# Kernel tuning notes

Hardware: AMD Instinct MI355X
Metric: run time of the kernel (lower is better)

Reference implementation:

```python
import jax, jax.numpy as jnp
import numpy as np

N_QUBITS = 6
BLOCKS = 3
LATENT = 3
DIM = 1 << N_QUBITS  # 64, state-vector size
BATCH = 131072
INP_DIM = 6  # must equal N_QUBITS (repo applies linear_pre to the n_qubits-dim recon)

# Wire 0 is the most-significant qubit (PennyLane convention).
_idx = np.arange(DIM)
BITS = ((_idx[:, None] >> (N_QUBITS - 1 - np.arange(N_QUBITS))) & 1)  # (64, 6)
# Chain of CZ(k, k+1): all diagonal, fold into one sign vector per block.
CZ_SIGN = jnp.asarray(np.prod(1 - 2 * (BITS[:, :-1] * BITS[:, 1:]), axis=1).astype(np.float32))  # (64,)
Z_SIGNS = jnp.asarray((1 - 2 * BITS).astype(np.float32))  # (64, 6): <Z_k> signs per basis state


def _apply_1q(state, U, wire):
    # state: (B, 64) complex64; U: (2,2) complex64 acting on `wire`
    B = state.shape[0]
    s = state.reshape(B, 1 << wire, 2, 1 << (N_QUBITS - 1 - wire))
    s = jnp.einsum('ij,bxjy->bxiy', U, s)
    return s.reshape(B, DIM)


def _circuit(amps, weights, n_out):
    # AmplitudeEmbedding with normalize=True (x was already unit-normed in torch; idempotent)
    norm = jnp.linalg.norm(amps, axis=1, keepdims=True)
    state = (amps / norm).astype(jnp.complex64)  # (B, 64)
    for j in range(BLOCKS):
        for k in range(N_QUBITS):
            tx = weights[j, k, 0]
            tz = weights[j, k, 1]
            c = jnp.cos(0.5 * tx).astype(jnp.complex64)
            s = jnp.sin(0.5 * tx).astype(jnp.complex64)
            em = jnp.exp(-0.5j * tz).astype(jnp.complex64)
            ep = jnp.exp(0.5j * tz).astype(jnp.complex64)
            # Fused U = RZ(tz) @ RX(tx)
            U = jnp.stack([jnp.stack([em * c, -1j * em * s]),
                           jnp.stack([-1j * ep * s, ep * c])])
            state = _apply_1q(state, U, k)
        state = state * CZ_SIGN  # all CZ gates of the block, fused
    probs = state.real ** 2 + state.imag ** 2  # (B, 64)
    return probs @ Z_SIGNS[:, :n_out]  # expval(PauliZ(k)) for k < n_out


def setup_inputs() -> dict:
    key = jax.random.key(0)
    k1, k2, k3, k4, k5 = jax.random.split(key, 5)
    x = jax.random.normal(k1, (BATCH, INP_DIM), dtype=jnp.float32)
    bound = 1.0 / np.sqrt(INP_DIM)
    W_pre = jax.random.uniform(k2, (DIM, INP_DIM), minval=-bound, maxval=bound, dtype=jnp.float32)
    b_pre = jax.random.uniform(k3, (DIM,), minval=-bound, maxval=bound, dtype=jnp.float32)
    enc_w = jax.random.normal(k4, (BLOCKS, N_QUBITS, 3), dtype=jnp.float32) * 0.01
    dec_w = jax.random.normal(k5, (BLOCKS, N_QUBITS, 3), dtype=jnp.float32) * 0.01
    return {'x': x, 'W_pre': W_pre, 'b_pre': b_pre, 'enc_w': enc_w, 'dec_w': dec_w}


def reference(x, W_pre, b_pre, enc_w, dec_w):
    h = jnp.tanh(x @ W_pre.T + b_pre)                     # (B, 64)
    latent = _circuit(h, enc_w, LATENT)                    # (B, 3)
    padded = jnp.zeros((x.shape[0], DIM), jnp.float32).at[:, :LATENT].set(latent)
    recon = _circuit(padded, dec_w, N_QUBITS)              # (B, 6)
    reconstructed = jnp.tanh(recon @ W_pre.T + b_pre)      # (B, 64)
    return reconstructed, latent
```

## Files before the change

kernel.cpp:

```cpp
#include <hip/hip_runtime.h>

#define BATCH 131072

typedef float v2f __attribute__((ext_vector_type(2)));


__device__ __forceinline__ float fast_tanh(float v) {
    float e = __expf(2.0f * v);
    return 1.0f - 2.0f / (e + 1.0f);
}

template <int CTRL>
__device__ __forceinline__ float dppf(float v) {
    return __int_as_float(__builtin_amdgcn_update_dpp(
        0, __float_as_int(v), CTRL, 0xF, 0xF, true));
}
#define DPP_XOR1 0xB1
#define DPP_XOR2 0x4E

__device__ __forceinline__ v2f swap2(v2f v) { return __builtin_shufflevector(v, v, 1, 0); }

__global__ __launch_bounds__(256) void prep_kernel(const float* __restrict__ enc_w,
                                                   const float* __restrict__ dec_w,
                                                   const float* __restrict__ Wp,
                                                   const float* __restrict__ bp,
                                                   float* __restrict__ ws) {
    __shared__ float gt[18][8];
    __shared__ float Sr[64][8];
    __shared__ float Si[64][8];
    __shared__ float sA[36];
    const int t = threadIdx.x;

    if (t < 18) {
        float tx = dec_w[t * 3 + 0];
        float tz = dec_w[t * 3 + 1];
        float c = cosf(0.5f * tx), s = sinf(0.5f * tx);
        float ch = cosf(0.5f * tz), sh = sinf(0.5f * tz);
        gt[t][0] = c * ch;  gt[t][1] = -c * sh;
        gt[t][2] = -s * sh; gt[t][3] = -s * ch;
        gt[t][4] = s * sh;  gt[t][5] = -s * ch;
        gt[t][6] = c * ch;  gt[t][7] = c * sh;
    }

    const int cl = t & 7;
    const int pr = t >> 3;
    float* fSr = &Sr[0][0];
    float* fSi = &Si[0][0];
    for (int f = t; f < 512; f += 256) {
        int r = f >> 3, c = f & 7;
        fSr[f] = (r == c && c < 3) ? 1.0f : 0.0f;
        fSi[f] = 0.0f;
    }

    for (int bb = 0; bb < 3; ++bb) {
        for (int w = 0; w < 6; ++w) {
            __syncthreads();
            int g = bb * 6 + w;
            int p = 5 - w;
            float u00r = gt[g][0], u00i = gt[g][1], u01r = gt[g][2], u01i = gt[g][3];
            float u10r = gt[g][4], u10i = gt[g][5], u11r = gt[g][6], u11i = gt[g][7];
            int r0 = ((pr >> p) << (p + 1)) | (pr & ((1 << p) - 1));
            int r1 = r0 | (1 << p);
            float ar = Sr[r0][cl], ai = Si[r0][cl];
            float br = Sr[r1][cl], bi = Si[r1][cl];
            Sr[r0][cl] = u00r * ar - u00i * ai + u01r * br - u01i * bi;
            Si[r0][cl] = u00r * ai + u00i * ar + u01r * bi + u01i * br;
            Sr[r1][cl] = u10r * ar - u10i * ai + u11r * br - u11i * bi;
            Si[r1][cl] = u10r * ai + u10i * ar + u11r * bi + u11i * br;
        }
        __syncthreads();
        for (int f = t; f < 512; f += 256) {
            int r = f >> 3;
            if (__popc(r & (r >> 1)) & 1) {
                fSr[f] = -fSr[f];
                fSi[f] = -fSi[f];
            }
        }
    }
    __syncthreads();

    if (t < 36) {
        int k = t / 6, i = t % 6;
        int d = (i < 3) ? i : ((i == 5) ? 1 : 0);
        int e = (i < 3) ? i : ((i == 3) ? 1 : 2);
        float acc = 0.0f;
        for (int r = 0; r < 64; ++r) {
            float term = Sr[r][d] * Sr[r][e] + Si[r][d] * Si[r][e];
            acc += ((r >> (5 - k)) & 1) ? -term : term;
        }
        if (i >= 3) acc *= 2.0f;
        sA[t] = acc;
    }

    if (t < 18) {
        float tx = enc_w[t * 3 + 0];
        float c = cosf(0.5f * tx), s = sinf(0.5f * tx);
        if (t >= 12) {
            ws[64 + 2 * t] = c * c - s * s;
            ws[65 + 2 * t] = 4.0f * c * s;
        } else {
            ws[64 + 2 * t] = c;
            ws[65 + 2 * t] = s;
        }
    }

    if (t >= 64 && t < 256) {
        int idx = t - 64;
        int bb = idx >> 6, r = idx & 63;
        float phi = 0.0f;
        for (int k = 0; k < 6; ++k) {
            float tz = enc_w[(bb * 6 + k) * 3 + 1];
            phi += ((r >> (5 - k)) & 1) ? 0.5f * tz : -0.5f * tz;
        }
        float sgn = (__popc(r & (r >> 1)) & 1) ? -1.0f : 1.0f;
        ws[128 + bb * 128 + 2 * r] = sgn * cosf(phi);
        ws[129 + bb * 128 + 2 * r] = sgn * sinf(phi);
    }
    __syncthreads();

    if (t < 64) {
        float w0 = Wp[t * 6 + 0], w1 = Wp[t * 6 + 1], w2 = Wp[t * 6 + 2];
        float w3 = Wp[t * 6 + 3], w4 = Wp[t * 6 + 4], w5 = Wp[t * 6 + 5];
#pragma unroll
        for (int i = 0; i < 6; ++i) {
            float acc = w0 * sA[0 * 6 + i] + w1 * sA[1 * 6 + i] + w2 * sA[2 * 6 + i]
                      + w3 * sA[3 * 6 + i] + w4 * sA[4 * 6 + i] + w5 * sA[5 * 6 + i];
            ws[512 + t * 8 + i] = acc;
        }
        ws[512 + t * 8 + 6] = bp[t];
        ws[512 + t * 8 + 7] = 0.0f;
    }
}

template <int MASK>
__device__ __forceinline__ void rx_pairs(v2f* zr, v2f* zi, float c, float s) {
#pragma unroll
    for (int j = 0; j < 8; ++j) {
        if (j & MASK) continue;
        int j1 = j | MASK;
        v2f ar = zr[j], ai = zi[j], br = zr[j1], bi = zi[j1];
        zr[j]  = c * ar + s * bi;
        zi[j]  = c * ai - s * br;
        zr[j1] = c * br + s * ai;
        zi[j1] = c * bi - s * ar;
    }
}

template <int CTRL>
__device__ __forceinline__ void rx_exch2(v2f* zr, v2f* zi, float c, float s) {
#pragma unroll
    for (int j = 0; j < 8; ++j) {
        v2f pr, pi;
        pr.x = dppf<CTRL>(zr[j].x);
        pr.y = dppf<CTRL>(zr[j].y);
        pi.x = dppf<CTRL>(zi[j].x);
        pi.y = dppf<CTRL>(zi[j].y);
        v2f mr = zr[j], mi = zi[j];
        zr[j] = c * mr + s * pi;
        zi[j] = c * mi - s * pr;
    }
}

__device__ __forceinline__ void enc_tail(v2f* zr, v2f* zi, const float* rx,
                                         const float* sDblk, int sub) {
    rx_pairs<2>(zr, zi, rx[2], rx[3]);
    rx_pairs<1>(zr, zi, rx[4], rx[5]);
    {
        float c = rx[6], s = rx[7];
#pragma unroll
        for (int j = 0; j < 8; ++j) {
            v2f orr = zr[j], oi = zi[j];
            zr[j] = c * orr + s * swap2(oi);
            zi[j] = c * oi - s * swap2(orr);
        }
    }
    rx_exch2<DPP_XOR2>(zr, zi, rx[8], rx[9]);
    rx_exch2<DPP_XOR1>(zr, zi, rx[10], rx[11]);
#pragma unroll
    for (int j = 0; j < 8; ++j) {
        float4 d = *(const float4*)&sDblk[(j * 4 + sub) * 4];
        v2f dr = {d.x, d.y}, di = {d.z, d.w};
        v2f orr = zr[j], oi = zi[j];
        zr[j] = dr * orr - di * oi;
        zi[j] = dr * oi + di * orr;
    }
}

__global__ __launch_bounds__(256, 4) void qae_main(const float* __restrict__ x,
                                                   const float* __restrict__ Wp,
                                                   const float* __restrict__ bp,
                                                   const float* __restrict__ ws,
                                                   float* __restrict__ out) {
    __shared__ float sW[540];
    __shared__ float sB[544];
    __shared__ float sD[256];

    const int t = threadIdx.x;
    const int bl = t >> 2;
    const int sub = t & 3;

    const size_t b = (size_t)blockIdx.x * 64 + bl;
    const float* xp = x + b * 6;
    float2 x01 = *(const float2*)(xp);
    float2 x23 = *(const float2*)(xp + 2);
    float2 x45 = *(const float2*)(xp + 4);

    for (int f = t; f < 512; f += 256) {
        int g = f >> 4, e = f & 15;
        int j = g >> 2, su = g & 3;
        float val;
        if (e < 12)      { int row = 8 * j + su + 4 * (e & 1); val = Wp[row * 6 + (e >> 1)]; }
        else if (e < 14) { int row = 8 * j + su + 4 * (e - 12); val = bp[row]; }
        else val = 0.0f;
        sW[g * 16 + j * 4 + e] = val;
    }
    for (int f = t; f < 512; f += 256) {
        sB[f + ((f >> 7) << 2)] = ws[512 + f];
    }
    if (t < 128) {
        int bb = t >> 6, r = t & 63;
        int su = r & 3, m = r >> 2, j = m >> 1, hm = m & 1;
        int base = ((bb * 8 + j) * 4 + su) * 4;
        sD[base + hm]     = ws[128 + bb * 128 + 2 * r];
        sD[base + 2 + hm] = ws[128 + bb * 128 + 2 * r + 1];
    }
    __syncthreads();

    float xv[6] = {x01.x, x01.y, x23.x, x23.y, x45.x, x45.y};

    v2f zr[8], zi[8];
    v2f S2 = {0.0f, 0.0f};
#pragma unroll
    for (int j = 0; j < 8; ++j) {
        const float* wb = &sW[(j * 4 + sub) * 16 + j * 4];
        float4 c0 = *(const float4*)wb;
        float4 c1 = *(const float4*)(wb + 4);
        float4 c2 = *(const float4*)(wb + 8);
        float4 c3 = *(const float4*)(wb + 12);
        v2f a = {c3.x, c3.y};
        a += xv[0] * (v2f){c0.x, c0.y};
        a += xv[1] * (v2f){c0.z, c0.w};
        a += xv[2] * (v2f){c1.x, c1.y};
        a += xv[3] * (v2f){c1.z, c1.w};
        a += xv[4] * (v2f){c2.x, c2.y};
        a += xv[5] * (v2f){c2.z, c2.w};
        v2f th = {fast_tanh(a.x), fast_tanh(a.y)};
        zr[j] = th;
        S2 += th * th;
    }
    float S = S2.x + S2.y;
    S += dppf<DPP_XOR1>(S);
    S += dppf<DPP_XOR2>(S);
    float invS = __builtin_amdgcn_rcpf(S);

    {
        const float* rx = ws + 64;
        float c = rx[0], s = rx[1];
#pragma unroll
        for (int j = 0; j < 4; ++j) {
            v2f a = zr[j], b2 = zr[j + 4];
            zr[j]     = c * a;
            zi[j]     = -s * b2;
            zr[j + 4] = c * b2;
            zi[j + 4] = -s * a;
        }
        enc_tail(zr, zi, rx, sD, sub);
    }
    {
        const float* rx = ws + 76;
        rx_pairs<4>(zr, zi, rx[0], rx[1]);
        enc_tail(zr, zi, rx, sD + 128, sub);
    }

    v2f L0 = {0, 0}, L1 = {0, 0}, L2 = {0, 0};
#pragma unroll
    for (int j = 0; j < 8; ++j) {
        v2f p = zr[j] * zr[j] + zi[j] * zi[j];
        L0 += (j & 4) ? -p : p;
        L1 += (j & 2) ? -p : p;
        L2 += (j & 1) ? -p : p;
    }
    v2f Y0 = {0, 0}, Y1 = {0, 0}, Y2 = {0, 0};
#pragma unroll
    for (int j = 0; j < 4; ++j)
        Y0 += zr[j] * zi[j | 4] - zi[j] * zr[j | 4];
#pragma unroll
    for (int j0 = 0; j0 < 8; j0 += 4)
#pragma unroll
        for (int j = j0; j < j0 + 2; ++j)
            Y1 += zr[j] * zi[j | 2] - zi[j] * zr[j | 2];
#pragma unroll
    for (int j = 0; j < 8; j += 2)
        Y2 += zr[j] * zi[j | 1] - zi[j] * zr[j | 1];

    const float* p2 = ws + 88;
    float t0 = p2[0] * (L0.x + L0.y) + p2[1] * (Y0.x + Y0.y);
    float t1 = p2[2] * (L1.x + L1.y) + p2[3] * (Y1.x + Y1.y);
    float t2 = p2[4] * (L2.x + L2.y) + p2[5] * (Y2.x + Y2.y);
    t0 += dppf<DPP_XOR1>(t0); t0 += dppf<DPP_XOR2>(t0);
    t1 += dppf<DPP_XOR1>(t1); t1 += dppf<DPP_XOR2>(t1);
    t2 += dppf<DPP_XOR1>(t2); t2 += dppf<DPP_XOR2>(t2);
    float l0 = t0 * invS, l1 = t1 * invS, l2 = t2 * invS;

    if (sub == 0) {
        size_t lo = (size_t)BATCH * 64 + b * 3;
        out[lo]     = l0;
        out[lo + 1] = l1;
        out[lo + 2] = l2;
    }

    float q0 = l0 * l0, q1 = l1 * l1, q2 = l2 * l2;
    float invr2 = __builtin_amdgcn_rcpf(q0 + q1 + q2);
    float qh0 = q0 * invr2, qh1 = q1 * invr2, qh2 = q2 * invr2;
    float qh3 = (l0 * l1) * invr2, qh4 = (l0 * l2) * invr2, qh5 = (l1 * l2) * invr2;

    const float* bB = &sB[132 * sub];
    const size_t ob = b * 64 + 16 * sub;
#pragma unroll
    for (int ch = 0; ch < 4; ++ch) {
        float v4[4];
#pragma unroll
        for (int r = 0; r < 4; ++r) {
            int qq = ch * 4 + r;
            float4 u0 = *(const float4*)&bB[8 * qq];
            float4 u1 = *(const float4*)&bB[8 * qq + 4];
            float acc = u1.z
                      + qh0 * u0.x + qh1 * u0.y + qh2 * u0.z + qh3 * u0.w
                      + qh4 * u1.x + qh5 * u1.y;
            v4[r] = fast_tanh(acc);
        }
        float4 o = {v4[0], v4[1], v4[2], v4[3]};
        *(float4*)&out[ob + ch * 4] = o;
    }
}

extern "C" void kernel_launch(void* const* d_in, const int* in_sizes, int n_in,
                              void* d_out, int out_size, void* d_ws, size_t ws_size,
                              hipStream_t stream) {
    const float* x   = (const float*)d_in[0];
    const float* Wp  = (const float*)d_in[1];
    const float* bpv = (const float*)d_in[2];
    const float* enc = (const float*)d_in[3];
    const float* dec = (const float*)d_in[4];
    float* out = (float*)d_out;
    float* ws  = (float*)d_ws;

    prep_kernel<<<1, 256, 0, stream>>>(enc, dec, Wp, bpv, ws);
    qae_main<<<(BATCH * 4) / 256, 256, 0, stream>>>(x, Wp, bpv, ws, out);
}
```

Measured before the change: 102.2 us.

## Fuse parameter prep kernel into main kernel, recomputing per block

Removes the separate single-block prep kernel and its workspace round-trip. Each block of the main kernel now recomputes the decoder circuit's observable matrix, the encoder rotation constants and the diagonal phase tables in shared memory, reusing one aliased shared buffer. This saves a kernel launch and the serial dependency on a one-block kernel. In exchange every one of the 2048 blocks redoes the prep work, including about 20 __syncthreads and transcendental calls, before it starts its batch work.

```diff
diff --git a/kernel.cpp b/kernel.cpp
--- a/kernel.cpp
+++ b/kernel.cpp
@@ -3,7 +3,6 @@
 #define BATCH 131072
 
 typedef float v2f __attribute__((ext_vector_type(2)));
-
 
 __device__ __forceinline__ float fast_tanh(float v) {
     float e = __expf(2.0f * v);
@@ -19,118 +18,6 @@
 #define DPP_XOR2 0x4E
 
 __device__ __forceinline__ v2f swap2(v2f v) { return __builtin_shufflevector(v, v, 1, 0); }
-
-__global__ __launch_bounds__(256) void prep_kernel(const float* __restrict__ enc_w,
-                                                   const float* __restrict__ dec_w,
-                                                   const float* __restrict__ Wp,
-                                                   const float* __restrict__ bp,
-                                                   float* __restrict__ ws) {
-    __shared__ float gt[18][8];
-    __shared__ float Sr[64][8];
-    __shared__ float Si[64][8];
-    __shared__ float sA[36];
-    const int t = threadIdx.x;
-
-    if (t < 18) {
-        float tx = dec_w[t * 3 + 0];
-        float tz = dec_w[t * 3 + 1];
-        float c = cosf(0.5f * tx), s = sinf(0.5f * tx);
-        float ch = cosf(0.5f * tz), sh = sinf(0.5f * tz);
-        gt[t][0] = c * ch;  gt[t][1] = -c * sh;
-        gt[t][2] = -s * sh; gt[t][3] = -s * ch;
-        gt[t][4] = s * sh;  gt[t][5] = -s * ch;
-        gt[t][6] = c * ch;  gt[t][7] = c * sh;
-    }
-
-    const int cl = t & 7;
-    const int pr = t >> 3;
-    float* fSr = &Sr[0][0];
-    float* fSi = &Si[0][0];
-    for (int f = t; f < 512; f += 256) {
-        int r = f >> 3, c = f & 7;
-        fSr[f] = (r == c && c < 3) ? 1.0f : 0.0f;
-        fSi[f] = 0.0f;
-    }
-
-    for (int bb = 0; bb < 3; ++bb) {
-        for (int w = 0; w < 6; ++w) {
-            __syncthreads();
-            int g = bb * 6 + w;
-            int p = 5 - w;
-            float u00r = gt[g][0], u00i = gt[g][1], u01r = gt[g][2], u01i = gt[g][3];
-            float u10r = gt[g][4], u10i = gt[g][5], u11r = gt[g][6], u11i = gt[g][7];
-            int r0 = ((pr >> p) << (p + 1)) | (pr & ((1 << p) - 1));
-            int r1 = r0 | (1 << p);
-            float ar = Sr[r0][cl], ai = Si[r0][cl];
-            float br = Sr[r1][cl], bi = Si[r1][cl];
-            Sr[r0][cl] = u00r * ar - u00i * ai + u01r * br - u01i * bi;
-            Si[r0][cl] = u00r * ai + u00i * ar + u01r * bi + u01i * br;
-            Sr[r1][cl] = u10r * ar - u10i * ai + u11r * br - u11i * bi;
-            Si[r1][cl] = u10r * ai + u10i * ar + u11r * bi + u11i * br;
-        }
-        __syncthreads();
-        for (int f = t; f < 512; f += 256) {
-            int r = f >> 3;
-            if (__popc(r & (r >> 1)) & 1) {
-                fSr[f] = -fSr[f];
-                fSi[f] = -fSi[f];
-            }
-        }
-    }
-    __syncthreads();
-
-    if (t < 36) {
-        int k = t / 6, i = t % 6;
-        int d = (i < 3) ? i : ((i == 5) ? 1 : 0);
-        int e = (i < 3) ? i : ((i == 3) ? 1 : 2);
-        float acc = 0.0f;
-        for (int r = 0; r < 64; ++r) {
-            float term = Sr[r][d] * Sr[r][e] + Si[r][d] * Si[r][e];
-            acc += ((r >> (5 - k)) & 1) ? -term : term;
-        }
-        if (i >= 3) acc *= 2.0f;
-        sA[t] = acc;
-    }
-
-    if (t < 18) {
-        float tx = enc_w[t * 3 + 0];
-        float c = cosf(0.5f * tx), s = sinf(0.5f * tx);
-        if (t >= 12) {
-            ws[64 + 2 * t] = c * c - s * s;
-            ws[65 + 2 * t] = 4.0f * c * s;
-        } else {
-            ws[64 + 2 * t] = c;
-            ws[65 + 2 * t] = s;
-        }
-    }
-
-    if (t >= 64 && t < 256) {
-        int idx = t - 64;
-        int bb = idx >> 6, r = idx & 63;
-        float phi = 0.0f;
-        for (int k = 0; k < 6; ++k) {
-            float tz = enc_w[(bb * 6 + k) * 3 + 1];
-            phi += ((r >> (5 - k)) & 1) ? 0.5f * tz : -0.5f * tz;
-        }
-        float sgn = (__popc(r & (r >> 1)) & 1) ? -1.0f : 1.0f;
-        ws[128 + bb * 128 + 2 * r] = sgn * cosf(phi);
-        ws[129 + bb * 128 + 2 * r] = sgn * sinf(phi);
-    }
-    __syncthreads();
-
-    if (t < 64) {
-        float w0 = Wp[t * 6 + 0], w1 = Wp[t * 6 + 1], w2 = Wp[t * 6 + 2];
-        float w3 = Wp[t * 6 + 3], w4 = Wp[t * 6 + 4], w5 = Wp[t * 6 + 5];
-#pragma unroll
-        for (int i = 0; i < 6; ++i) {
-            float acc = w0 * sA[0 * 6 + i] + w1 * sA[1 * 6 + i] + w2 * sA[2 * 6 + i]
-                      + w3 * sA[3 * 6 + i] + w4 * sA[4 * 6 + i] + w5 * sA[5 * 6 + i];
-            ws[512 + t * 8 + i] = acc;
-        }
-        ws[512 + t * 8 + 6] = bp[t];
-        ws[512 + t * 8 + 7] = 0.0f;
-    }
-}
 
 template <int MASK>
 __device__ __forceinline__ void rx_pairs(v2f* zr, v2f* zi, float c, float s) {
@@ -186,14 +73,22 @@
     }
 }
 
-__global__ __launch_bounds__(256, 4) void qae_main(const float* __restrict__ x,
-                                                   const float* __restrict__ Wp,
-                                                   const float* __restrict__ bp,
-                                                   const float* __restrict__ ws,
-                                                   float* __restrict__ out) {
-    __shared__ float sW[540];
-    __shared__ float sB[544];
-    __shared__ float sD[256];
+__global__ __launch_bounds__(256, 4) void qae_fused(const float* __restrict__ x,
+                                                    const float* __restrict__ Wp,
+                                                    const float* __restrict__ bp,
+                                                    const float* __restrict__ enc_w,
+                                                    const float* __restrict__ dec_w,
+                                                    float* __restrict__ out) {
+    __shared__ __align__(16) float shbuf[1344];
+    __shared__ float sA[36];
+    __shared__ float sRx[36];
+
+    float* gt = shbuf;
+    float* Sr = shbuf + 144;
+    float* Si = shbuf + 656;
+    float* sW = shbuf;
+    float* sB = shbuf + 544;
+    float* sD = shbuf + 1088;
 
     const int t = threadIdx.x;
     const int bl = t >> 2;
@@ -204,6 +99,74 @@
     float2 x01 = *(const float2*)(xp);
     float2 x23 = *(const float2*)(xp + 2);
     float2 x45 = *(const float2*)(xp + 4);
+
+    if (t < 18) {
+        float tx = dec_w[t * 3 + 0];
+        float tz = dec_w[t * 3 + 1];
+        float c = cosf(0.5f * tx), s = sinf(0.5f * tx);
+        float ch = cosf(0.5f * tz), sh = sinf(0.5f * tz);
+        gt[t * 8 + 0] = c * ch;  gt[t * 8 + 1] = -c * sh;
+        gt[t * 8 + 2] = -s * sh; gt[t * 8 + 3] = -s * ch;
+        gt[t * 8 + 4] = s * sh;  gt[t * 8 + 5] = -s * ch;
+        gt[t * 8 + 6] = c * ch;  gt[t * 8 + 7] = c * sh;
+        float etx = enc_w[t * 3 + 0];
+        float ec = cosf(0.5f * etx), es = sinf(0.5f * etx);
+        if (t >= 12) {
+            sRx[2 * t] = ec * ec - es * es;
+            sRx[2 * t + 1] = 4.0f * ec * es;
+        } else {
+            sRx[2 * t] = ec;
+            sRx[2 * t + 1] = es;
+        }
+    }
+    const int cl = t & 7;
+    const int pr = t >> 3;
+    for (int f = t; f < 512; f += 256) {
+        int r = f >> 3, c = f & 7;
+        Sr[f] = (r == c && c < 3) ? 1.0f : 0.0f;
+        Si[f] = 0.0f;
+    }
+
+    for (int bb = 0; bb < 3; ++bb) {
+        for (int w = 0; w < 6; ++w) {
+            __syncthreads();
+            int g = bb * 6 + w;
+            int p = 5 - w;
+            float u00r = gt[g * 8 + 0], u00i = gt[g * 8 + 1], u01r = gt[g * 8 + 2], u01i = gt[g * 8 + 3];
+            float u10r = gt[g * 8 + 4], u10i = gt[g * 8 + 5], u11r = gt[g * 8 + 6], u11i = gt[g * 8 + 7];
+            int r0 = ((pr >> p) << (p + 1)) | (pr & ((1 << p) - 1));
+            int r1 = r0 | (1 << p);
+            float ar = Sr[r0 * 8 + cl], ai = Si[r0 * 8 + cl];
+            float br = Sr[r1 * 8 + cl], bi = Si[r1 * 8 + cl];
+            Sr[r0 * 8 + cl] = u00r * ar - u00i * ai + u01r * br - u01i * bi;
+            Si[r0 * 8 + cl] = u00r * ai + u00i * ar + u01r * bi + u01i * br;
+            Sr[r1 * 8 + cl] = u10r * ar - u10i * ai + u11r * br - u11i * bi;
+            Si[r1 * 8 + cl] = u10r * ai + u10i * ar + u11r * bi + u11i * br;
+        }
+        __syncthreads();
+        for (int f = t; f < 512; f += 256) {
+            int r = f >> 3;
+            if (__popc(r & (r >> 1)) & 1) {
+                Sr[f] = -Sr[f];
+                Si[f] = -Si[f];
+            }
+        }
+    }
+    __syncthreads();
+
+    if (t < 36) {
+        int k = t / 6, i = t % 6;
+        int d = (i < 3) ? i : ((i == 5) ? 1 : 0);
+        int e = (i < 3) ? i : ((i == 3) ? 1 : 2);
+        float acc = 0.0f;
+        for (int r = 0; r < 64; ++r) {
+            float term = Sr[r * 8 + d] * Sr[r * 8 + e] + Si[r * 8 + d] * Si[r * 8 + e];
+            acc += ((r >> (5 - k)) & 1) ? -term : term;
+        }
+        if (i >= 3) acc *= 2.0f;
+        sA[t] = acc;
+    }
+    __syncthreads();
 
     for (int f = t; f < 512; f += 256) {
         int g = f >> 4, e = f & 15;
@@ -214,15 +177,32 @@
         else val = 0.0f;
         sW[g * 16 + j * 4 + e] = val;
     }
-    for (int f = t; f < 512; f += 256) {
-        sB[f + ((f >> 7) << 2)] = ws[512 + f];
-    }
-    if (t < 128) {
-        int bb = t >> 6, r = t & 63;
+    if (t < 64) {
+        float w0 = Wp[t * 6 + 0], w1 = Wp[t * 6 + 1], w2 = Wp[t * 6 + 2];
+        float w3 = Wp[t * 6 + 3], w4 = Wp[t * 6 + 4], w5 = Wp[t * 6 + 5];
+        int basep = 8 * t + ((t >> 4) << 2);
+#pragma unroll
+        for (int i = 0; i < 6; ++i) {
+            float acc = w0 * sA[0 * 6 + i] + w1 * sA[1 * 6 + i] + w2 * sA[2 * 6 + i]
+                      + w3 * sA[3 * 6 + i] + w4 * sA[4 * 6 + i] + w5 * sA[5 * 6 + i];
+            sB[basep + i] = acc;
+        }
+        sB[basep + 6] = bp[t];
+        sB[basep + 7] = 0.0f;
+    }
+    if (t >= 64 && t < 192) {
+        int idx = t - 64;
+        int bb = idx >> 6, r = idx & 63;
+        float phi = 0.0f;
+        for (int k = 0; k < 6; ++k) {
+            float tz = enc_w[(bb * 6 + k) * 3 + 1];
+            phi += ((r >> (5 - k)) & 1) ? 0.5f * tz : -0.5f * tz;
+        }
+        float sgn = (__popc(r & (r >> 1)) & 1) ? -1.0f : 1.0f;
         int su = r & 3, m = r >> 2, j = m >> 1, hm = m & 1;
         int base = ((bb * 8 + j) * 4 + su) * 4;
-        sD[base + hm]     = ws[128 + bb * 128 + 2 * r];
-        sD[base + 2 + hm] = ws[128 + bb * 128 + 2 * r + 1];
+        sD[base + hm]     = sgn * cosf(phi);
+        sD[base + 2 + hm] = sgn * sinf(phi);
     }
     __syncthreads();
 
@@ -254,7 +234,7 @@
     float invS = __builtin_amdgcn_rcpf(S);
 
     {
-        const float* rx = ws + 64;
+        const float* rx = sRx;
         float c = rx[0], s = rx[1];
 #pragma unroll
         for (int j = 0; j < 4; ++j) {
@@ -267,7 +247,7 @@
         enc_tail(zr, zi, rx, sD, sub);
     }
     {
-        const float* rx = ws + 76;
+        const float* rx = sRx + 12;
         rx_pairs<4>(zr, zi, rx[0], rx[1]);
         enc_tail(zr, zi, rx, sD + 128, sub);
     }
@@ -293,7 +273,7 @@
     for (int j = 0; j < 8; j += 2)
         Y2 += zr[j] * zi[j | 1] - zi[j] * zr[j | 1];
 
-    const float* p2 = ws + 88;
+    const float* p2 = sRx + 24;
     float t0 = p2[0] * (L0.x + L0.y) + p2[1] * (Y0.x + Y0.y);
     float t1 = p2[2] * (L1.x + L1.y) + p2[3] * (Y1.x + Y1.y);
     float t2 = p2[4] * (L2.x + L2.y) + p2[5] * (Y2.x + Y2.y);
@@ -343,8 +323,6 @@
     const float* enc = (const float*)d_in[3];
     const float* dec = (const float*)d_in[4];
     float* out = (float*)d_out;
-    float* ws  = (float*)d_ws;
-
-    prep_kernel<<<1, 256, 0, stream>>>(enc, dec, Wp, bpv, ws);
-    qae_main<<<(BATCH * 4) / 256, 256, 0, stream>>>(x, Wp, bpv, ws, out);
-}
+
+    qae_fused<<<(BATCH * 4) / 256, 256, 0, stream>>>(x, Wp, bpv, enc, dec, out);
+}
```

Result: no change. 102.6 us (+0.4%).
